# Performance work log

Hardware: AMD Instinct MI355X
Metric: run time of the kernel (lower is better)

## Reference

```python
import jax, jax.numpy as jnp
import numpy as np

N_HEAD = 16  # from __init__ default used at construction


def setup_inputs() -> dict:
    key = jax.random.key(0)
    k1, k2 = jax.random.split(key)
    b, c, h, w = 4, 320, 96, 192
    lf = jax.random.normal(k1, (b, c, h, w), dtype=jnp.float32)
    rf = jax.random.normal(k2, (b, c, h, w), dtype=jnp.float32)
    return {"lf": lf, "rf": rf, "d_max": 64}


def reference(lf, rf, d_max):
    b, c, h, w = lf.shape
    n_channels = c // N_HEAD
    # group the channel dim: [b, g, nc, h, w]
    lfg = lf.reshape(b, N_HEAD, n_channels, h, w)
    # left-pad rf with d_max zeros along width so a shift by d is a static-size
    # slice; zero padding reproduces the zero-filled region of the cost volume
    # (lf * 0 == 0 for x < d).
    rfp = jnp.pad(rf, ((0, 0), (0, 0), (0, 0), (d_max, 0)))
    rfp = rfp.reshape(b, N_HEAD, n_channels, h, w + d_max)

    def body(carry, d):
        # rf shifted right by d (positions x < d are zero)
        r_shift = jax.lax.dynamic_slice_in_dim(rfp, d_max - d, w, axis=4)
        # group-wise correlation: reduce over the per-group channel dim
        cost = jnp.einsum('bgchw,bgchw->bghw', lfg, r_shift)
        return carry, cost

    _, costs = jax.lax.scan(body, None, jnp.arange(d_max))  # [d_max, b, g, h, w]
    disp_block = jnp.transpose(costs, (1, 2, 0, 3, 4))       # [b, g, d_max, h, w]
    return disp_block / np.float32(np.sqrt(n_channels))
```

## Files before the change

kernel.cpp:

```cpp
#include <hip/hip_runtime.h>

#define BSZ   4
#define CCH   320
#define HH    96
#define WW    192
#define NHEAD 16
#define NC    20
#define DMAX  64
#define HWSZ  (HH * WW)
#define NSLOT (WW + DMAX)
#define SPAD  12
#define NROW  2
#define TPR   96

typedef _Float16 half2v __attribute__((ext_vector_type(2)));
typedef float    f32x2  __attribute__((ext_vector_type(2)));
#define BC(u) __builtin_bit_cast(half2v, u)

__global__ __launch_bounds__(192) void gwc_kernel(const float* __restrict__ lf,
                                                  const float* __restrict__ rf,
                                                  float* __restrict__ out) {
    __shared__ __align__(16) unsigned int rfs[NROW][NSLOT][SPAD];

    const int tid = threadIdx.x;
    const int r   = tid / TPR;
    const int i   = tid % TPR;
    int bid = blockIdx.x;
    const int yp = bid % (HH / NROW); bid /= (HH / NROW);
    const int bg = bid;
    const int y0 = yp * NROW;

    for (int k = tid; k < NROW * DMAX * SPAD; k += 192) {
        const int rr  = k / (DMAX * SPAD);
        const int off = k % (DMAX * SPAD);
        (&rfs[rr][0][0])[off] = 0u;
    }

    const size_t gbase = (size_t)bg * NC * HWSZ;

    for (int it = tid; it < NROW * WW; it += 192) {
        const int rr = it / WW, x = it % WW;
        const float* rp = rf + gbase + (size_t)(y0 + rr) * WW + x;
        unsigned int w[10];
#pragma unroll
        for (int j = 0; j < 10; ++j) {
            const float v0 = rp[(size_t)(2 * j) * HWSZ];
            const float v1 = rp[(size_t)(2 * j + 1) * HWSZ];
            w[j] = __builtin_bit_cast(unsigned int, half2v{(_Float16)v0, (_Float16)v1});
        }
        unsigned int* dst = &rfs[rr][DMAX + x][0];
        *(uint4*)(dst + 0) = make_uint4(w[0], w[1], w[2], w[3]);
        *(uint4*)(dst + 4) = make_uint4(w[4], w[5], w[6], w[7]);
        *(uint2*)(dst + 8) = make_uint2(w[8], w[9]);
    }

    half2v L0[10], L1[10];
    {
        const float* lp = lf + gbase + (size_t)(y0 + r) * WW + 2 * i;
#pragma unroll
        for (int j = 0; j < 10; ++j) {
            const float2 c0 = *(const float2*)(lp + (size_t)(2 * j) * HWSZ);
            const float2 c1 = *(const float2*)(lp + (size_t)(2 * j + 1) * HWSZ);
            L0[j] = half2v{(_Float16)c0.x, (_Float16)c1.x};
            L1[j] = half2v{(_Float16)c0.y, (_Float16)c1.y};
        }
    }
    __syncthreads();

    const float scale = 0.22360679774997896f;
    float* op = out + (size_t)bg * DMAX * HWSZ + (size_t)(y0 + r) * WW + 2 * i;
    const unsigned int (*buf)[SPAD] = rfs[r];

#pragma unroll 4
    for (int d = 0; d < DMAX; ++d) {
        const unsigned int* pA = &buf[2 * i + DMAX - d][0];
        const uint4 a0 = *(const uint4*)(pA + 0);
        const uint4 a1 = *(const uint4*)(pA + 4);
        const uint2 a2 = *(const uint2*)(pA + 8);
        const uint4 b0 = *(const uint4*)(pA + SPAD + 0);
        const uint4 b1 = *(const uint4*)(pA + SPAD + 4);
        const uint2 b2 = *(const uint2*)(pA + SPAD + 8);

        float sa = 0.f, sb = 0.f, ta = 0.f, tb = 0.f;
        sa = __builtin_amdgcn_fdot2(L0[0], BC(a0.x), sa, false);
        sb = __builtin_amdgcn_fdot2(L0[1], BC(a0.y), sb, false);
        sa = __builtin_amdgcn_fdot2(L0[2], BC(a0.z), sa, false);
        sb = __builtin_amdgcn_fdot2(L0[3], BC(a0.w), sb, false);
        sa = __builtin_amdgcn_fdot2(L0[4], BC(a1.x), sa, false);
        sb = __builtin_amdgcn_fdot2(L0[5], BC(a1.y), sb, false);
        sa = __builtin_amdgcn_fdot2(L0[6], BC(a1.z), sa, false);
        sb = __builtin_amdgcn_fdot2(L0[7], BC(a1.w), sb, false);
        sa = __builtin_amdgcn_fdot2(L0[8], BC(a2.x), sa, false);
        sb = __builtin_amdgcn_fdot2(L0[9], BC(a2.y), sb, false);
        ta = __builtin_amdgcn_fdot2(L1[0], BC(b0.x), ta, false);
        tb = __builtin_amdgcn_fdot2(L1[1], BC(b0.y), tb, false);
        ta = __builtin_amdgcn_fdot2(L1[2], BC(b0.z), ta, false);
        tb = __builtin_amdgcn_fdot2(L1[3], BC(b0.w), tb, false);
        ta = __builtin_amdgcn_fdot2(L1[4], BC(b1.x), ta, false);
        tb = __builtin_amdgcn_fdot2(L1[5], BC(b1.y), tb, false);
        ta = __builtin_amdgcn_fdot2(L1[6], BC(b1.z), ta, false);
        tb = __builtin_amdgcn_fdot2(L1[7], BC(b1.w), tb, false);
        ta = __builtin_amdgcn_fdot2(L1[8], BC(b2.x), ta, false);
        tb = __builtin_amdgcn_fdot2(L1[9], BC(b2.y), tb, false);

        const f32x2 v = {(sa + sb) * scale, (ta + tb) * scale};
        __builtin_nontemporal_store(v, (f32x2*)(op + (size_t)d * HWSZ));
    }
}

extern "C" void kernel_launch(void* const* d_in, const int* in_sizes, int n_in,
                              void* d_out, int out_size, void* d_ws, size_t ws_size,
                              hipStream_t stream) {
    const float* lf = (const float*)d_in[0];
    const float* rf = (const float*)d_in[1];
    float* out = (float*)d_out;

    const int grid = BSZ * NHEAD * (HH / NROW);
    gwc_kernel<<<grid, 192, 0, stream>>>(lf, rf, out);
}
```

Before: 78.14 us.

## Split shared rf rows by parity and reuse each LDS load across adjacent disparities

Stores right-feature columns in separate even and odd shared-memory planes. Each LDS vector read now serves two outputs: the even pixel at disparity d and the odd pixel at disparity d+1, with the second result carried into the next iteration. This halves LDS read traffic per output. The block also grows to 4 rows and 384 threads, which halves the grid size and raises per-block shared memory.

```diff
diff --git a/kernel.cpp b/kernel.cpp
--- a/kernel.cpp
+++ b/kernel.cpp
@@ -8,19 +8,34 @@
 #define NC    20
 #define DMAX  64
 #define HWSZ  (HH * WW)
-#define NSLOT (WW + DMAX)
 #define SPAD  12
-#define NROW  2
+#define NROW  4
 #define TPR   96
+#define NTHR  (NROW * TPR)
 
 typedef _Float16 half2v __attribute__((ext_vector_type(2)));
 typedef float    f32x2  __attribute__((ext_vector_type(2)));
 #define BC(u) __builtin_bit_cast(half2v, u)
 
-__global__ __launch_bounds__(192) void gwc_kernel(const float* __restrict__ lf,
-                                                  const float* __restrict__ rf,
-                                                  float* __restrict__ out) {
-    __shared__ __align__(16) unsigned int rfs[NROW][NSLOT][SPAD];
+__device__ __forceinline__ float dot20h(const half2v* L, uint4 a0, uint4 a1, uint2 a2) {
+    float sa = 0.f, sb = 0.f;
+    sa = __builtin_amdgcn_fdot2(L[0], BC(a0.x), sa, false);
+    sb = __builtin_amdgcn_fdot2(L[1], BC(a0.y), sb, false);
+    sa = __builtin_amdgcn_fdot2(L[2], BC(a0.z), sa, false);
+    sb = __builtin_amdgcn_fdot2(L[3], BC(a0.w), sb, false);
+    sa = __builtin_amdgcn_fdot2(L[4], BC(a1.x), sa, false);
+    sb = __builtin_amdgcn_fdot2(L[5], BC(a1.y), sb, false);
+    sa = __builtin_amdgcn_fdot2(L[6], BC(a1.z), sa, false);
+    sb = __builtin_amdgcn_fdot2(L[7], BC(a1.w), sb, false);
+    sa = __builtin_amdgcn_fdot2(L[8], BC(a2.x), sa, false);
+    sb = __builtin_amdgcn_fdot2(L[9], BC(a2.y), sb, false);
+    return sa + sb;
+}
+
+__global__ __launch_bounds__(NTHR) void gwc_kernel(const float* __restrict__ lf,
+                                                   const float* __restrict__ rf,
+                                                   float* __restrict__ out) {
+    __shared__ __align__(16) unsigned int rfs[NROW][2][128][SPAD];
 
     const int tid = threadIdx.x;
     const int r   = tid / TPR;
@@ -30,15 +45,17 @@
     const int bg = bid;
     const int y0 = yp * NROW;
 
-    for (int k = tid; k < NROW * DMAX * SPAD; k += 192) {
-        const int rr  = k / (DMAX * SPAD);
-        const int off = k % (DMAX * SPAD);
-        (&rfs[rr][0][0])[off] = 0u;
+    for (int k = tid; k < NROW * 2 * 32 * SPAD; k += NTHR) {
+        const int rr  = k / (2 * 32 * SPAD);
+        const int rem = k % (2 * 32 * SPAD);
+        const int par = rem / (32 * SPAD);
+        const int off = rem % (32 * SPAD);
+        (&rfs[rr][par][0][0])[off] = 0u;
     }
 
     const size_t gbase = (size_t)bg * NC * HWSZ;
 
-    for (int it = tid; it < NROW * WW; it += 192) {
+    for (int it = tid; it < NROW * WW; it += NTHR) {
         const int rr = it / WW, x = it % WW;
         const float* rp = rf + gbase + (size_t)(y0 + rr) * WW + x;
         unsigned int w[10];
@@ -48,7 +65,7 @@
             const float v1 = rp[(size_t)(2 * j + 1) * HWSZ];
             w[j] = __builtin_bit_cast(unsigned int, half2v{(_Float16)v0, (_Float16)v1});
         }
-        unsigned int* dst = &rfs[rr][DMAX + x][0];
+        unsigned int* dst = &rfs[rr][x & 1][(x >> 1) + 32][0];
         *(uint4*)(dst + 0) = make_uint4(w[0], w[1], w[2], w[3]);
         *(uint4*)(dst + 4) = make_uint4(w[4], w[5], w[6], w[7]);
         *(uint2*)(dst + 8) = make_uint2(w[8], w[9]);
@@ -69,42 +86,38 @@
 
     const float scale = 0.22360679774997896f;
     float* op = out + (size_t)bg * DMAX * HWSZ + (size_t)(y0 + r) * WW + 2 * i;
-    const unsigned int (*buf)[SPAD] = rfs[r];
+    const unsigned int (*E)[SPAD] = rfs[r][0];
+    const unsigned int (*O)[SPAD] = rfs[r][1];
 
-#pragma unroll 4
-    for (int d = 0; d < DMAX; ++d) {
-        const unsigned int* pA = &buf[2 * i + DMAX - d][0];
-        const uint4 a0 = *(const uint4*)(pA + 0);
-        const uint4 a1 = *(const uint4*)(pA + 4);
-        const uint2 a2 = *(const uint2*)(pA + 8);
-        const uint4 b0 = *(const uint4*)(pA + SPAD + 0);
-        const uint4 b1 = *(const uint4*)(pA + SPAD + 4);
-        const uint2 b2 = *(const uint2*)(pA + SPAD + 8);
+    float ocarry;
+    {
+        const unsigned int* p = &O[i + 32][0];
+        ocarry = dot20h(L1, *(const uint4*)(p + 0), *(const uint4*)(p + 4),
+                        *(const uint2*)(p + 8)) * scale;
+    }
 
-        float sa = 0.f, sb = 0.f, ta = 0.f, tb = 0.f;
-        sa = __builtin_amdgcn_fdot2(L0[0], BC(a0.x), sa, false);
-        sb = __builtin_amdgcn_fdot2(L0[1], BC(a0.y), sb, false);
-        sa = __builtin_amdgcn_fdot2(L0[2], BC(a0.z), sa, false);
-        sb = __builtin_amdgcn_fdot2(L0[3], BC(a0.w), sb, false);
-        sa = __builtin_amdgcn_fdot2(L0[4], BC(a1.x), sa, false);
-        sb = __builtin_amdgcn_fdot2(L0[5], BC(a1.y), sb, false);
-        sa = __builtin_amdgcn_fdot2(L0[6], BC(a1.z), sa, false);
-        sb = __builtin_amdgcn_fdot2(L0[7], BC(a1.w), sb, false);
-        sa = __builtin_amdgcn_fdot2(L0[8], BC(a2.x), sa, false);
-        sb = __builtin_amdgcn_fdot2(L0[9], BC(a2.y), sb, false);
-        ta = __builtin_amdgcn_fdot2(L1[0], BC(b0.x), ta, false);
-        tb = __builtin_amdgcn_fdot2(L1[1], BC(b0.y), tb, false);
-        ta = __builtin_amdgcn_fdot2(L1[2], BC(b0.z), ta, false);
-        tb = __builtin_amdgcn_fdot2(L1[3], BC(b0.w), tb, false);
-        ta = __builtin_amdgcn_fdot2(L1[4], BC(b1.x), ta, false);
-        tb = __builtin_amdgcn_fdot2(L1[5], BC(b1.y), tb, false);
-        ta = __builtin_amdgcn_fdot2(L1[6], BC(b1.z), ta, false);
-        tb = __builtin_amdgcn_fdot2(L1[7], BC(b1.w), tb, false);
-        ta = __builtin_amdgcn_fdot2(L1[8], BC(b2.x), ta, false);
-        tb = __builtin_amdgcn_fdot2(L1[9], BC(b2.y), tb, false);
-
-        const f32x2 v = {(sa + sb) * scale, (ta + tb) * scale};
-        __builtin_nontemporal_store(v, (f32x2*)(op + (size_t)d * HWSZ));
+#pragma unroll 2
+    for (int t = 0; t < 32; ++t) {
+        {
+            const unsigned int* p = &E[i + 32 - t][0];
+            const uint4 a0 = *(const uint4*)(p + 0);
+            const uint4 a1 = *(const uint4*)(p + 4);
+            const uint2 a2 = *(const uint2*)(p + 8);
+            const float e = dot20h(L0, a0, a1, a2) * scale;
+            __builtin_nontemporal_store((f32x2){e, ocarry},
+                                        (f32x2*)(op + (size_t)(2 * t) * HWSZ));
+            ocarry = dot20h(L1, a0, a1, a2) * scale;
+        }
+        {
+            const unsigned int* p = &O[i + 31 - t][0];
+            const uint4 a0 = *(const uint4*)(p + 0);
+            const uint4 a1 = *(const uint4*)(p + 4);
+            const uint2 a2 = *(const uint2*)(p + 8);
+            const float e = dot20h(L0, a0, a1, a2) * scale;
+            __builtin_nontemporal_store((f32x2){e, ocarry},
+                                        (f32x2*)(op + (size_t)(2 * t + 1) * HWSZ));
+            ocarry = dot20h(L1, a0, a1, a2) * scale;
+        }
     }
 }
 
@@ -116,5 +129,5 @@
     float* out = (float*)d_out;
 
     const int grid = BSZ * NHEAD * (HH / NROW);
-    gwc_kernel<<<grid, 192, 0, stream>>>(lf, rf, out);
+    gwc_kernel<<<grid, NTHR, 0, stream>>>(lf, rf, out);
 }
```

Measured after the change: 81.27 us. 1.04x slower.
